# Optimization experiments

Measured on AMD Instinct MI355X. Metric: run time of the kernel, lower is better.

## Reference

```python
import jax, jax.numpy as jnp
import numpy as np

BINS = 30
MOMENTUM = 0.75  # first call: last_bin_count is None, so momentum has no effect


def setup_inputs() -> dict:
    key = jax.random.key(0)
    k1, k2 = jax.random.split(key)
    logits = jax.random.normal(k1, (4096, 8192), dtype=jnp.float32)
    target = jax.random.randint(k2, (4096, 8192), 0, 2, dtype=jnp.int32)
    return {"logits": logits, "target": target}


def reference(logits, target):
    t = target.astype(logits.dtype)
    # gradient-density statistic (detached in torch)
    g = jnp.abs(jax.nn.sigmoid(jax.lax.stop_gradient(logits)) - t)
    bin_idx = jnp.floor(g * (BINS - 0.0001)).astype(jnp.int32)  # in [0, BINS-1]
    # histogram over bins (single fused scatter-add, no per-bin host sync)
    flat_idx = bin_idx.reshape(-1)
    bin_count = jax.ops.segment_sum(
        jnp.ones_like(flat_idx, dtype=logits.dtype), flat_idx, num_segments=BINS
    )
    nonempty_bins = jnp.sum(bin_count > 0).astype(logits.dtype)
    tot = jnp.asarray(logits.size, dtype=logits.dtype)
    beta = tot / jnp.clip(bin_count * nonempty_bins, 1e-4)  # [BINS]
    weight = beta[bin_idx]  # gather per-element weight
    # binary_cross_entropy_with_logits, reduction='none', weighted
    bce = -(t * jax.nn.log_sigmoid(logits) + (1.0 - t) * jax.nn.log_sigmoid(-logits))
    loss = weight * bce
    return loss.mean(axis=1)
```

## Files before the change

kernel.cpp:

```cpp
#include <hip/hip_runtime.h>
#include <math.h>

#define BINS 30
#define ROWS 4096
#define COLS 8192
#define REP  8
#define GREP 32
#define WSTK 64

__device__ __forceinline__ int bin_ref_f32(float x, int t)
{
    float e   = (float)exp(-(double)x);
    float d   = 1.0f + e;
    float sig = 1.0f / d;
    float g   = fabsf(sig - (float)t);
    float u   = g * 29.9999f;
    int b = (int)u;
    return b > (BINS - 1) ? (BINS - 1) : b;
}

__global__ __launch_bounds__(256, 4) void k_hist(const float* __restrict__ logits,
                                                 const int*   __restrict__ target,
                                                 float*       __restrict__ rowsum,
                                                 unsigned int* __restrict__ ghist)
{
    __shared__ unsigned int h[4][REP * BINS];
    __shared__ unsigned int sx[4][WSTK];
    __shared__ unsigned int sm[4][WSTK];
    __shared__ unsigned int scnt[4];

    const int tid  = threadIdx.x;
    const int wid  = tid >> 6;
    const int lane = tid & 63;
    const int row  = blockIdx.x * 4 + wid;

    unsigned int* hw = h[wid];
    #pragma unroll
    for (int i = lane; i < REP * BINS; i += 64) hw[i] = 0u;
    if (lane == 0) scnt[wid] = 0u;

    const int base = (lane & (REP - 1)) * BINS;
    const float4* lp = (const float4*)(logits + (size_t)row * COLS);
    const int4*   tp = (const int4*)(target + (size_t)row * COLS);

    for (int j = 0; j < 4; ++j) {
        float4 xv[8];
        int4   tv[8];
        #pragma unroll
        for (int k = 0; k < 8; ++k) {
            xv[k] = lp[lane + (j * 8 + k) * 64];
            tv[k] = tp[lane + (j * 8 + k) * 64];
        }
        #pragma unroll
        for (int k = 0; k < 8; ++k) {
            float xs[4] = {xv[k].x, xv[k].y, xv[k].z, xv[k].w};
            int   ts[4] = {tv[k].x, tv[k].y, tv[k].z, tv[k].w};
            #pragma unroll
            for (int c = 0; c < 4; ++c) {
                float s = __uint_as_float(__float_as_uint(xs[c]) ^
                                          ((unsigned int)ts[c] << 31));
                float z   = __builtin_amdgcn_exp2f(fabsf(s) * -1.44269504088896340736f);
                float d   = 1.0f + z;
                float inv = __builtin_amdgcn_rcpf(d);
                float g   = (s >= 0.0f) ? inv : z * inv;
                float bce = fmaf(__builtin_amdgcn_logf(d),
                                 0.69314718055994530942f, fmaxf(s, 0.0f));
                float u   = g * 29.9999f;
                int   bin = (int)u;
                unsigned int q = (unsigned int)fmaf(bce, 1024.0f, 0.5f);

                if (fabsf(u - rintf(u)) <= 5e-4f) {
                    unsigned int idx = atomicAdd(&scnt[wid], 1u);
                    if (idx < WSTK) {
                        sx[wid][idx] = __float_as_uint(xs[c]);
                        sm[wid][idx] = q | ((unsigned int)ts[c] << 21);
                    }
                } else {
                    atomicAdd(&hw[base + bin], (1u << 23) | q);
                }
            }
        }
    }

    unsigned int n = scnt[wid];
    n = n < WSTK ? n : WSTK;
    if (lane < (int)n) {
        float x = __uint_as_float(sx[wid][lane]);
        unsigned int mw = sm[wid][lane];
        int bin = bin_ref_f32(x, (int)(mw >> 21));
        atomicAdd(&hw[(lane & (REP - 1)) * BINS + bin],
                  (1u << 23) | (mw & 0x1FFFFFu));
    }

    if (lane < BINS) {
        unsigned int cnt = 0u;
        float        fs  = 0.0f;
        #pragma unroll
        for (int r = 0; r < REP; ++r) {
            unsigned int v = hw[r * BINS + lane];
            cnt += v >> 23;
            fs  += (float)(v & 0x7FFFFFu);
        }
        rowsum[(size_t)row * BINS + lane] = fs * (1.0f / 1024.0f);
        atomicAdd(&ghist[(row & (GREP - 1)) * 32 + lane], cnt);
    }
}

__global__ __launch_bounds__(256) void k_finish(const unsigned int* __restrict__ ghist,
                                                const float* __restrict__ rowsum,
                                                float* __restrict__ out)
{
    __shared__ float sb[BINS];
    const int tid = threadIdx.x;
    if (tid < 64) {
        const int b = tid;
        unsigned int c = 0u;
        if (b < BINS) {
            #pragma unroll
            for (int r = 0; r < GREP; ++r) c += ghist[r * 32 + b];
        }
        unsigned long long m = __ballot(b < BINS && c > 0u);
        float nonempty = (float)__popcll(m);
        if (b < BINS) {
            const float tot = (float)ROWS * (float)COLS;
            sb[b] = tot / fmaxf((float)c * nonempty, 1e-4f);
        }
    }
    __syncthreads();
    const int row = blockIdx.x * 256 + tid;
    const float* rp = rowsum + (size_t)row * BINS;
    float acc = 0.0f;
    #pragma unroll
    for (int b = 0; b < BINS; ++b) acc += sb[b] * rp[b];
    out[row] = acc * (1.0f / (float)COLS);
}

extern "C" void kernel_launch(void* const* d_in, const int* in_sizes, int n_in,
                              void* d_out, int out_size, void* d_ws, size_t ws_size,
                              hipStream_t stream)
{
    const float* logits = (const float*)d_in[0];
    const int*   target = (const int*)d_in[1];
    float*       out    = (float*)d_out;

    unsigned int* ghist  = (unsigned int*)d_ws;
    float*        rowsum = (float*)d_ws + GREP * 32;

    hipMemsetAsync(d_ws, 0, GREP * 32 * sizeof(unsigned int), stream);

    k_hist  <<<ROWS / 4, 256, 0, stream>>>(logits, target, rowsum, ghist);
    k_finish<<<ROWS / 256, 256, 0, stream>>>(ghist, rowsum, out);
}
```

Before: 54.97 us.

## Replace per-element sigmoid/log with LDS lookup table for softplus and bin

Adds a table-generation kernel that precomputes softplus values, fp16 slopes and bin indices over 4096 cells of the signed logit. The histogram kernel copies this table into LDS and uses linear interpolation plus a table bin lookup instead of exp/rcp/log per element. Elements in ambiguous bin cells or outside the table range are deferred to an exact slow path. Blocks grow to 512 threads. The aim is to cut transcendental ALU work, at the cost of an extra launch, LDS table loads and interpolation accuracy risk.

```diff
diff --git a/kernel.cpp b/kernel.cpp
--- a/kernel.cpp
+++ b/kernel.cpp
@@ -1,12 +1,15 @@
 #include <hip/hip_runtime.h>
+#include <hip/hip_fp16.h>
 #include <math.h>
 
-#define BINS 30
-#define ROWS 4096
-#define COLS 8192
-#define REP  8
-#define GREP 32
-#define WSTK 64
+#define BINS  30
+#define ROWS  4096
+#define COLS  8192
+#define GREP  32
+#define WSTK  256
+#define CELLS 4096
+#define TSCALE 322.519684f
+#define TOFF   2048.0f
 
 __device__ __forceinline__ int bin_ref_f32(float x, int t)
 {
@@ -19,84 +22,120 @@
     return b > (BINS - 1) ? (BINS - 1) : b;
 }
 
-__global__ __launch_bounds__(256, 4) void k_hist(const float* __restrict__ logits,
+__device__ __forceinline__ double softplus_f64(double s)
+{
+    return (s > 0.0) ? s + log1p(exp(-s)) : log1p(exp(s));
+}
+
+__global__ __launch_bounds__(256) void k_tabgen(unsigned int* __restrict__ gtab)
+{
+    const int i = blockIdx.x * 256 + threadIdx.x;
+    const double sc = (double)CELLS / 12.7;
+    double s_lo = ((double)i - 2048.0) / sc;
+    double s_hi = ((double)i + 1.0 - 2048.0) / sc;
+    double wl = s_lo - 0.01 / sc, wh = s_hi + 0.01 / sc;
+
+    float v0 = (float)softplus_f64(s_lo);
+    float sl = (float)(softplus_f64(s_hi) - softplus_f64(s_lo));
+
+    int b0a = bin_ref_f32((float)wl, 0), b0b = bin_ref_f32((float)wh, 0);
+    int b1a = bin_ref_f32(-(float)wl, 1), b1b = bin_ref_f32(-(float)wh, 1);
+    bool uni = (b0a == b0b) && (b1a == b1b) && (b0a == b1a);
+    unsigned int bb = (unsigned int)b0a | (uni ? 0u : 0x80u);
+
+    __half hs = __float2half(sl);
+    gtab[2 * i]     = __float_as_uint(v0);
+    gtab[2 * i + 1] = (unsigned int)__half_as_ushort(hs) | (bb << 16);
+}
+
+__global__ __launch_bounds__(512, 2) void k_hist(const float* __restrict__ logits,
                                                  const int*   __restrict__ target,
+                                                 const unsigned int* __restrict__ gtab,
                                                  float*       __restrict__ rowsum,
                                                  unsigned int* __restrict__ ghist)
 {
-    __shared__ unsigned int h[4][REP * BINS];
-    __shared__ unsigned int sx[4][WSTK];
-    __shared__ unsigned int sm[4][WSTK];
-    __shared__ unsigned int scnt[4];
+    __shared__ uint2        ltab[CELLS];
+    __shared__ unsigned int h[8][8 * BINS];
+    __shared__ unsigned int sx[8][WSTK];
+    __shared__ unsigned int sm[8][WSTK];
+    __shared__ unsigned int scnt[8];
 
     const int tid  = threadIdx.x;
     const int wid  = tid >> 6;
     const int lane = tid & 63;
-    const int row  = blockIdx.x * 4 + wid;
+    const int row  = blockIdx.x * 8 + wid;
 
+    #pragma unroll
+    for (int i = tid; i < CELLS / 2; i += 512)
+        ((uint4*)ltab)[i] = ((const uint4*)gtab)[i];
     unsigned int* hw = h[wid];
     #pragma unroll
-    for (int i = lane; i < REP * BINS; i += 64) hw[i] = 0u;
+    for (int i = lane; i < 8 * BINS; i += 64) hw[i] = 0u;
     if (lane == 0) scnt[wid] = 0u;
+    __syncthreads();
 
-    const int base = (lane & (REP - 1)) * BINS;
+    const int base = (lane & 7) * BINS;
     const float4* lp = (const float4*)(logits + (size_t)row * COLS);
     const int4*   tp = (const int4*)(target + (size_t)row * COLS);
 
-    for (int j = 0; j < 4; ++j) {
-        float4 xv[8];
-        int4   tv[8];
+    for (int j = 0; j < 16; ++j) {
+        float4 xv0 = lp[lane + (j * 2 + 0) * 64];
+        float4 xv1 = lp[lane + (j * 2 + 1) * 64];
+        int4   tv0 = tp[lane + (j * 2 + 0) * 64];
+        int4   tv1 = tp[lane + (j * 2 + 1) * 64];
+        float xs[8] = {xv0.x, xv0.y, xv0.z, xv0.w, xv1.x, xv1.y, xv1.z, xv1.w};
+        int   ts[8] = {tv0.x, tv0.y, tv0.z, tv0.w, tv1.x, tv1.y, tv1.z, tv1.w};
         #pragma unroll
-        for (int k = 0; k < 8; ++k) {
-            xv[k] = lp[lane + (j * 8 + k) * 64];
-            tv[k] = tp[lane + (j * 8 + k) * 64];
-        }
-        #pragma unroll
-        for (int k = 0; k < 8; ++k) {
-            float xs[4] = {xv[k].x, xv[k].y, xv[k].z, xv[k].w};
-            int   ts[4] = {tv[k].x, tv[k].y, tv[k].z, tv[k].w};
-            #pragma unroll
-            for (int c = 0; c < 4; ++c) {
-                float s = __uint_as_float(__float_as_uint(xs[c]) ^
-                                          ((unsigned int)ts[c] << 31));
-                float z   = __builtin_amdgcn_exp2f(fabsf(s) * -1.44269504088896340736f);
-                float d   = 1.0f + z;
-                float inv = __builtin_amdgcn_rcpf(d);
-                float g   = (s >= 0.0f) ? inv : z * inv;
-                float bce = fmaf(__builtin_amdgcn_logf(d),
-                                 0.69314718055994530942f, fmaxf(s, 0.0f));
-                float u   = g * 29.9999f;
-                int   bin = (int)u;
-                unsigned int q = (unsigned int)fmaf(bce, 1024.0f, 0.5f);
+        for (int c = 0; c < 8; ++c) {
+            float s = __uint_as_float(__float_as_uint(xs[c]) ^
+                                      ((unsigned int)ts[c] << 31));
+            float fidx = fmaf(s, TSCALE, TOFF);
+            float fcl  = fminf(fmaxf(fidx, 0.0f), 4095.0f);
+            int   idx  = (int)fcl;
+            float frac = fcl - (float)idx;
+            uint2 e = ltab[idx];
+            float slope = __half2float(__ushort_as_half((unsigned short)(e.y & 0xFFFFu)));
+            float bce   = fmaf(slope, frac, __uint_as_float(e.x));
+            unsigned int bb = (e.y >> 16) & 0xFFu;
+            unsigned int qf = (unsigned int)fmaf(bce, 1024.0f, 8388608.0f);
 
-                if (fabsf(u - rintf(u)) <= 5e-4f) {
-                    unsigned int idx = atomicAdd(&scnt[wid], 1u);
-                    if (idx < WSTK) {
-                        sx[wid][idx] = __float_as_uint(xs[c]);
-                        sm[wid][idx] = q | ((unsigned int)ts[c] << 21);
-                    }
+            bool defer = (bb > 127u) || (fabsf(fidx - TOFF) >= 2047.0f);
+            if (defer) {
+                unsigned int k = atomicAdd(&scnt[wid], 1u);
+                if (k < WSTK) {
+                    sx[wid][k] = __float_as_uint(xs[c]);
+                    sm[wid][k] = (qf & 0x7FFFFFu) | ((unsigned int)ts[c] << 31);
                 } else {
-                    atomicAdd(&hw[base + bin], (1u << 23) | q);
+                    int bin = bin_ref_f32(xs[c], ts[c]);
+                    atomicAdd(&hw[base + bin], qf);
                 }
+            } else {
+                atomicAdd(&hw[base + bb], qf);
             }
         }
     }
 
     unsigned int n = scnt[wid];
     n = n < WSTK ? n : WSTK;
-    if (lane < (int)n) {
-        float x = __uint_as_float(sx[wid][lane]);
-        unsigned int mw = sm[wid][lane];
-        int bin = bin_ref_f32(x, (int)(mw >> 21));
-        atomicAdd(&hw[(lane & (REP - 1)) * BINS + bin],
-                  (1u << 23) | (mw & 0x1FFFFFu));
+    for (unsigned int i = lane; i < n; i += 64) {
+        float x = __uint_as_float(sx[wid][i]);
+        unsigned int mw = sm[wid][i];
+        int t = (int)(mw >> 31);
+        float s = __uint_as_float(__float_as_uint(x) ^ ((unsigned int)t << 31));
+        float z   = __builtin_amdgcn_exp2f(fabsf(s) * -1.44269504088896340736f);
+        float inv = __builtin_amdgcn_rcpf(1.0f + z);
+        float g   = (s >= 0.0f) ? inv : z * inv;
+        float u   = g * 29.9999f;
+        int bin   = (int)u;
+        if (fabsf(u - rintf(u)) <= 5e-4f) bin = bin_ref_f32(x, t);
+        atomicAdd(&hw[base + bin], (1u << 23) | (mw & 0x7FFFFFu));
     }
 
     if (lane < BINS) {
         unsigned int cnt = 0u;
         float        fs  = 0.0f;
         #pragma unroll
-        for (int r = 0; r < REP; ++r) {
+        for (int r = 0; r < 8; ++r) {
             unsigned int v = hw[r * BINS + lane];
             cnt += v >> 23;
             fs  += (float)(v & 0x7FFFFFu);
@@ -144,10 +183,12 @@
     float*       out    = (float*)d_out;
 
     unsigned int* ghist  = (unsigned int*)d_ws;
-    float*        rowsum = (float*)d_ws + GREP * 32;
+    unsigned int* gtab   = (unsigned int*)d_ws + GREP * 32;
+    float*        rowsum = (float*)d_ws + GREP * 32 + 2 * CELLS;
 
     hipMemsetAsync(d_ws, 0, GREP * 32 * sizeof(unsigned int), stream);
 
-    k_hist  <<<ROWS / 4, 256, 0, stream>>>(logits, target, rowsum, ghist);
+    k_tabgen<<<CELLS / 256, 256, 0, stream>>>(gtab);
+    k_hist  <<<ROWS / 8, 512, 0, stream>>>(logits, target, gtab, rowsum, ghist);
     k_finish<<<ROWS / 256, 256, 0, stream>>>(ghist, rowsum, out);
 }
```

New measurement: 60.16 us. +9.4%, slower.
